# Kernel optimization log

Measured on AMD Instinct MI355X. Metric: run time of the kernel, lower is better.

Reference implementation:

```python
import jax, jax.numpy as jnp
import numpy as np

B, H, W, C, WS, SS = 32, 192, 192, 64, 6, 3
NH, NW = H // WS, W // WS
EPS = 1e-5

def _ln(x, g, b):
    m = x.mean(-1, keepdims=True)
    v = ((x - m) ** 2).mean(-1, keepdims=True)
    return (x - m) * jax.lax.rsqrt(v + EPS) * g + b

def _block(x, Wm, bm, g, b):
    # Linear -> LayerNorm -> GELU (exact erf, matching torch nn.GELU); dropout inactive (eval)
    return jax.nn.gelu(_ln(x @ Wm + bm, g, b), approximate=False)

def _window_context(grid, Wt, bt, gt, bet):
    # partition into WSxWS windows and mean-pool per window: [B,NH,NW,C]
    pooled = grid.reshape(B, NH, WS, NW, WS, C).mean(axis=(2, 4))
    tok = _block(pooled, Wt, bt, gt, bet)           # token_proj
    # broadcast window summary back to pixel grid: [B,H,W,C]
    return jnp.repeat(jnp.repeat(tok, WS, axis=1), WS, axis=2)

def setup_inputs() -> dict:
    key = jax.random.key(0)
    ks = jax.random.split(key, 7)
    return {
        "h_pixel": jax.random.normal(ks[0], (B, H * W, C), jnp.float32),
        "token_W": jax.random.normal(ks[1], (C, C), jnp.float32) * 0.05,
        "token_b": jax.random.normal(ks[2], (C,), jnp.float32) * 0.05,
        "token_g": jnp.ones((C,), jnp.float32),
        "token_beta": jnp.zeros((C,), jnp.float32),
        "fuse_W": jax.random.normal(ks[3], (C, C), jnp.float32) * 0.05,
        "fuse_b": jax.random.normal(ks[4], (C,), jnp.float32) * 0.05,
        "fuse_g": jnp.ones((C,), jnp.float32),
        "fuse_beta": jnp.zeros((C,), jnp.float32),
        "out_W": jax.random.normal(ks[5], (C, C), jnp.float32) * 0.05,
        "out_b": jax.random.normal(ks[6], (C,), jnp.float32) * 0.05,
        "out_g": jnp.ones((C,), jnp.float32),
        "out_beta": jnp.zeros((C,), jnp.float32),
    }

def reference(h_pixel, token_W, token_b, token_g, token_beta,
              fuse_W, fuse_b, fuse_g, fuse_beta,
              out_W, out_b, out_g, out_beta):
    grid = h_pixel.reshape(B, H, W, C)
    reg = _window_context(grid, token_W, token_b, token_g, token_beta)
    shifted = _window_context(jnp.roll(grid, (-SS, -SS), (1, 2)),
                              token_W, token_b, token_g, token_beta)
    shifted = jnp.roll(shifted, (SS, SS), (1, 2))
    ctx = _block(reg + shifted, fuse_W, fuse_b, fuse_g, fuse_beta)   # fuse (sum merge)
    ctx = _block(ctx, out_W, out_b, out_g, out_beta)                 # out_proj
    return ctx.reshape(B, H * W, C)
```

## Files before the change

kernel.cpp:

```cpp
#include <hip/hip_runtime.h>
#include <math.h>


#define HH 192
#define WW 192
#define CC 64

__device__ __forceinline__ float gelu_exact(float x) {
    return 0.5f * x * (1.0f + erff(x * 0.70710678118654752440f));
}

__device__ __forceinline__ float bcast(float v, int k) {
    return __int_as_float(__builtin_amdgcn_readlane(__float_as_int(v), k));
}

__device__ __forceinline__ float matvec64(float m, const float* Wc, float bias) {
    float y0 = bias, y1 = 0.f, y2 = 0.f, y3 = 0.f;
#pragma unroll
    for (int k = 0; k < 64; k += 4) {
        y0 += bcast(m, k)     * Wc[k];
        y1 += bcast(m, k + 1) * Wc[k + 1];
        y2 += bcast(m, k + 2) * Wc[k + 2];
        y3 += bcast(m, k + 3) * Wc[k + 3];
    }
    return (y0 + y1) + (y2 + y3);
}

__device__ __forceinline__ float ln_gelu(float y, float g, float b) {
    float s1 = y, s2 = y * y;
#pragma unroll
    for (int off = 32; off > 0; off >>= 1) {
        s1 += __shfl_xor(s1, off, 64);
        s2 += __shfl_xor(s2, off, 64);
    }
    float m = s1 * (1.0f / 64.0f);
    float v = s2 * (1.0f / 64.0f) - m * m;
    v = v < 0.f ? 0.f : v;
    return gelu_exact((y - m) * rsqrtf(v + 1e-5f) * g + b);
}

extern "C" __global__ __launch_bounds__(256)
void k_blocksum(const float* __restrict__ h, float* __restrict__ S) {
    int bby = blockIdx.x;
    int b = bby >> 6, by = bby & 63;
    for (int item = threadIdx.x; item < 512; item += 256) {
        int bx = item >> 3;
        int c0 = (item & 7) * 8;
        float acc[8] = {0.f, 0.f, 0.f, 0.f, 0.f, 0.f, 0.f, 0.f};
#pragma unroll
        for (int dy = 0; dy < 3; ++dy) {
#pragma unroll
            for (int dx = 0; dx < 3; ++dx) {
                int y = by * 3 + dy, x = bx * 3 + dx;
                const float4* p = reinterpret_cast<const float4*>(
                    h + (((size_t)b * HH + y) * WW + x) * CC + c0);
                float4 v0 = p[0], v1 = p[1];
                acc[0] += v0.x; acc[1] += v0.y; acc[2] += v0.z; acc[3] += v0.w;
                acc[4] += v1.x; acc[5] += v1.y; acc[6] += v1.z; acc[7] += v1.w;
            }
        }
        float4* o = reinterpret_cast<float4*>(S + (((size_t)bby) * 64 + bx) * CC + c0);
        o[0] = make_float4(acc[0], acc[1], acc[2], acc[3]);
        o[1] = make_float4(acc[4], acc[5], acc[6], acc[7]);
    }
}

extern "C" __global__ __launch_bounds__(256)
void k_token(const float* __restrict__ S,
             const float* __restrict__ Wt, const float* __restrict__ bt,
             const float* __restrict__ gt, const float* __restrict__ bet,
             float* __restrict__ tok) {
    int lane = threadIdx.x & 63;
    int wg = blockIdx.x * 4 + (threadIdx.x >> 6);
    float Wc[64];
#pragma unroll
    for (int k = 0; k < 64; ++k) Wc[k] = Wt[k * 64 + lane];
    float bias = bt[lane], gg = gt[lane], bb = bet[lane];
    int row0 = wg * 16;
    for (int i = 0; i < 16; ++i) {
        int row = row0 + i;
        int mode = row >> 15;
        int r = row & 32767;
        int b = r >> 10, wy = (r >> 5) & 31, wx = r & 31;
        int r0, r1, c0, c1;
        if (mode == 0) { r0 = 2 * wy;     r1 = 2 * wy + 1;        c0 = 2 * wx;     c1 = 2 * wx + 1; }
        else           { r0 = 2 * wy + 1; r1 = (2 * wy + 2) & 63; c0 = 2 * wx + 1; c1 = (2 * wx + 2) & 63; }
        const float* Sb = S + (size_t)b * 64 * 64 * 64;
        float pooled = (Sb[(r0 * 64 + c0) * 64 + lane] + Sb[(r0 * 64 + c1) * 64 + lane] +
                        Sb[(r1 * 64 + c0) * 64 + lane] + Sb[(r1 * 64 + c1) * 64 + lane]) * (1.0f / 36.0f);
        float y = matvec64(pooled, Wc, bias);
        tok[(size_t)row * 64 + lane] = ln_gelu(y, gg, bb);
    }
}

extern "C" __global__ __launch_bounds__(256)
void k_fuse(const float* __restrict__ tok,
            const float* __restrict__ Wf, const float* __restrict__ bf_,
            const float* __restrict__ gf, const float* __restrict__ bef,
            float* __restrict__ h1) {
    int lane = threadIdx.x & 63;
    int wg = blockIdx.x * 4 + (threadIdx.x >> 6);
    float Wc[64];
#pragma unroll
    for (int k = 0; k < 64; ++k) Wc[k] = Wf[k * 64 + lane];
    float fb = bf_[lane], fg = gf[lane], fbe = bef[lane];
    int row0 = wg * 16;
    for (int i = 0; i < 16; ++i) {
        int row = row0 + i;
        int b = row >> 12;
        int rem = row & 4095;
        int wy = rem >> 7, wx = (rem >> 2) & 31, q = rem & 3;
        int sy = (wy + 31 + (q >> 1)) & 31;
        int sx = (wx + 31 + (q & 1)) & 31;
        const float* t0 = tok + (size_t)b * 65536;
        const float* t1 = tok + 2097152 + (size_t)b * 65536;
        float m = t0[(wy * 32 + wx) * 64 + lane] + t1[(sy * 32 + sx) * 64 + lane];
        float y = matvec64(m, Wc, fb);
        h1[(size_t)row * 64 + lane] = ln_gelu(y, fg, fbe);
    }
}

extern "C" __global__ __launch_bounds__(256)
void k_outbc(const float* __restrict__ h1,
             const float* __restrict__ Wo, const float* __restrict__ bo_,
             const float* __restrict__ go, const float* __restrict__ beo,
             float* __restrict__ out) {
    int lane = threadIdx.x & 63;
    int wg = blockIdx.x * 4 + (threadIdx.x >> 6);
    float Wc[64];
#pragma unroll
    for (int k = 0; k < 64; ++k) Wc[k] = Wo[k * 64 + lane];
    float ob = bo_[lane], og = go[lane], obe = beo[lane];
    int row0 = wg * 16;
    for (int i = 0; i < 16; ++i) {
        int row = row0 + i;
        float m = h1[(size_t)row * 64 + lane];
        float z = matvec64(m, Wc, ob);
        float o = ln_gelu(z, og, obe);
        int b = row >> 12;
        int rem = row & 4095;
        int wy = rem >> 7, wx = (rem >> 2) & 31, q = rem & 3;
        int y0 = wy * 6 + (q >> 1) * 3;
        int x0 = wx * 6 + (q & 1) * 3;
        float* obase = out + (((size_t)b * HH + y0) * WW + x0) * CC + lane;
#pragma unroll
        for (int dy = 0; dy < 3; ++dy) {
#pragma unroll
            for (int dx = 0; dx < 3; ++dx) {
                obase[((size_t)dy * WW + dx) * CC] = o;
            }
        }
    }
}

extern "C" void kernel_launch(void* const* d_in, const int* in_sizes, int n_in,
                              void* d_out, int out_size, void* d_ws, size_t ws_size,
                              hipStream_t stream) {
    const float* h   = (const float*)d_in[0];
    const float* tW  = (const float*)d_in[1];
    const float* tb  = (const float*)d_in[2];
    const float* tg  = (const float*)d_in[3];
    const float* tbe = (const float*)d_in[4];
    const float* fW  = (const float*)d_in[5];
    const float* fb  = (const float*)d_in[6];
    const float* fg  = (const float*)d_in[7];
    const float* fbe = (const float*)d_in[8];
    const float* oW  = (const float*)d_in[9];
    const float* ob  = (const float*)d_in[10];
    const float* og  = (const float*)d_in[11];
    const float* obe = (const float*)d_in[12];
    float* out = (float*)d_out;

    char* ws = (char*)d_ws;
    float* S   = (float*)(ws);
    float* tok = (float*)(ws + 33554432);
    float* h1  = S;

    hipLaunchKernelGGL(k_blocksum, dim3(2048), dim3(256), 0, stream, h, S);
    hipLaunchKernelGGL(k_token, dim3(1024), dim3(256), 0, stream,
                       S, tW, tb, tg, tbe, tok);
    hipLaunchKernelGGL(k_fuse, dim3(2048), dim3(256), 0, stream,
                       tok, fW, fb, fg, fbe, h1);
    hipLaunchKernelGGL(k_outbc, dim3(2048), dim3(256), 0, stream,
                       h1, oW, ob, og, obe, out);
}
```

Before: 622.2 us.

## Fold LayerNorm mean into centered weights and load activation rows via scalar loads

Adds a prep kernel that subtracts the per-row output-channel mean from each weight matrix and bias. This makes the linear output zero-mean, so LayerNorm only needs the variance reduction and half the cross-lane shuffles go away. The fuse and out kernels now fetch each 64-float input row with s_load_dwordx16 into scalar registers instead of broadcasting with readlane. The fuse kernel also reuses the regular-token partial matvec across the four shifted quadrants. The costs are an extra tiny launch, inline asm with a full lgkmcnt wait per row, and a more serialized scalar-load path.

```diff
diff --git a/kernel.cpp b/kernel.cpp
--- a/kernel.cpp
+++ b/kernel.cpp
@@ -6,12 +6,39 @@
 #define WW 192
 #define CC 64
 
+typedef __attribute__((ext_vector_type(16))) int i16v;
+
 __device__ __forceinline__ float gelu_exact(float x) {
     return 0.5f * x * (1.0f + erff(x * 0.70710678118654752440f));
 }
-
+__device__ __forceinline__ float wsum64(float v) {
+#pragma unroll
+    for (int off = 32; off > 0; off >>= 1) v += __shfl_xor(v, off, 64);
+    return v;
+}
 __device__ __forceinline__ float bcast(float v, int k) {
     return __int_as_float(__builtin_amdgcn_readlane(__float_as_int(v), k));
+}
+
+__device__ __forceinline__ void smem_row64(const float* rp,
+                                           i16v& a, i16v& b, i16v& c, i16v& d) {
+    asm volatile("s_load_dwordx16 %0, %4, 0x0\n\t"
+                 "s_load_dwordx16 %1, %4, 0x40\n\t"
+                 "s_load_dwordx16 %2, %4, 0x80\n\t"
+                 "s_load_dwordx16 %3, %4, 0xc0\n\t"
+                 "s_waitcnt lgkmcnt(0)"
+                 : "=&s"(a), "=&s"(b), "=&s"(c), "=&s"(d)
+                 : "s"(rp));
+}
+__device__ __forceinline__ void mac16(const i16v& a, const float* Wc, int base,
+                                      float& y0, float& y1, float& y2, float& y3) {
+#pragma unroll
+    for (int t = 0; t < 16; t += 4) {
+        y0 = fmaf(__int_as_float(a[t + 0]), Wc[base + t + 0], y0);
+        y1 = fmaf(__int_as_float(a[t + 1]), Wc[base + t + 1], y1);
+        y2 = fmaf(__int_as_float(a[t + 2]), Wc[base + t + 2], y2);
+        y3 = fmaf(__int_as_float(a[t + 3]), Wc[base + t + 3], y3);
+    }
 }
 
 __device__ __forceinline__ float matvec64(float m, const float* Wc, float bias) {
@@ -26,17 +53,31 @@
     return (y0 + y1) + (y2 + y3);
 }
 
-__device__ __forceinline__ float ln_gelu(float y, float g, float b) {
-    float s1 = y, s2 = y * y;
-#pragma unroll
-    for (int off = 32; off > 0; off >>= 1) {
-        s1 += __shfl_xor(s1, off, 64);
-        s2 += __shfl_xor(s2, off, 64);
-    }
-    float m = s1 * (1.0f / 64.0f);
-    float v = s2 * (1.0f / 64.0f) - m * m;
-    v = v < 0.f ? 0.f : v;
-    return gelu_exact((y - m) * rsqrtf(v + 1e-5f) * g + b);
+__device__ __forceinline__ float ln_gelu_c(float y, float g, float b) {
+    float s2 = y * y;
+#pragma unroll
+    for (int off = 32; off > 0; off >>= 1) s2 += __shfl_xor(s2, off, 64);
+    float v = s2 * (1.0f / 64.0f);
+    return gelu_exact(y * rsqrtf(v + 1e-5f) * g + b);
+}
+
+extern "C" __global__ __launch_bounds__(192)
+void k_prep(const float* __restrict__ W0, const float* __restrict__ b0,
+            const float* __restrict__ W1, const float* __restrict__ b1,
+            const float* __restrict__ W2, const float* __restrict__ b2,
+            float* __restrict__ cw) {
+    int lane = threadIdx.x & 63;
+    int w = threadIdx.x >> 6;
+    const float* W  = (w == 0) ? W0 : (w == 1) ? W1 : W2;
+    const float* bs = (w == 0) ? b0 : (w == 1) ? b1 : b2;
+    float* Wo = cw + w * 4096;
+    float* bo = cw + 12288 + w * 64;
+    for (int k = 0; k < 64; ++k) {
+        float v = W[k * 64 + lane];
+        Wo[k * 64 + lane] = v - wsum64(v) * (1.0f / 64.0f);
+    }
+    float bv = bs[lane];
+    bo[lane] = bv - wsum64(bv) * (1.0f / 64.0f);
 }
 
 extern "C" __global__ __launch_bounds__(256)
@@ -89,7 +130,7 @@
         float pooled = (Sb[(r0 * 64 + c0) * 64 + lane] + Sb[(r0 * 64 + c1) * 64 + lane] +
                         Sb[(r1 * 64 + c0) * 64 + lane] + Sb[(r1 * 64 + c1) * 64 + lane]) * (1.0f / 36.0f);
         float y = matvec64(pooled, Wc, bias);
-        tok[(size_t)row * 64 + lane] = ln_gelu(y, gg, bb);
+        tok[(size_t)row * 64 + lane] = ln_gelu_c(y, gg, bb);
     }
 }
 
@@ -99,24 +140,41 @@
             const float* __restrict__ gf, const float* __restrict__ bef,
             float* __restrict__ h1) {
     int lane = threadIdx.x & 63;
-    int wg = blockIdx.x * 4 + (threadIdx.x >> 6);
+    int wid = __builtin_amdgcn_readfirstlane(threadIdx.x >> 6);
+    int wg = blockIdx.x * 4 + wid;
     float Wc[64];
 #pragma unroll
     for (int k = 0; k < 64; ++k) Wc[k] = Wf[k * 64 + lane];
     float fb = bf_[lane], fg = gf[lane], fbe = bef[lane];
     int row0 = wg * 16;
-    for (int i = 0; i < 16; ++i) {
-        int row = row0 + i;
-        int b = row >> 12;
-        int rem = row & 4095;
-        int wy = rem >> 7, wx = (rem >> 2) & 31, q = rem & 3;
-        int sy = (wy + 31 + (q >> 1)) & 31;
-        int sx = (wx + 31 + (q & 1)) & 31;
-        const float* t0 = tok + (size_t)b * 65536;
-        const float* t1 = tok + 2097152 + (size_t)b * 65536;
-        float m = t0[(wy * 32 + wx) * 64 + lane] + t1[(sy * 32 + sx) * 64 + lane];
-        float y = matvec64(m, Wc, fb);
-        h1[(size_t)row * 64 + lane] = ln_gelu(y, fg, fbe);
+    int b = row0 >> 12;
+    int rem = row0 & 4095;
+    int wy = rem >> 7, wx0 = (rem >> 2) & 31;
+    const float* t0 = tok + (size_t)b * 65536;
+    const float* t1 = tok + 2097152 + (size_t)b * 65536;
+    for (int j = 0; j < 4; ++j) {
+        int wx = wx0 + j;
+        i16v a0, a1, a2, a3;
+        smem_row64(t0 + (wy * 32 + wx) * 64, a0, a1, a2, a3);
+        float s0 = fb, s1 = 0.f, s2 = 0.f, s3 = 0.f;
+        mac16(a0, Wc, 0, s0, s1, s2, s3);
+        mac16(a1, Wc, 16, s0, s1, s2, s3);
+        mac16(a2, Wc, 32, s0, s1, s2, s3);
+        mac16(a3, Wc, 48, s0, s1, s2, s3);
+#pragma unroll
+        for (int q = 0; q < 4; ++q) {
+            int sy = (wy + 31 + (q >> 1)) & 31;
+            int sx = (wx + 31 + (q & 1)) & 31;
+            i16v b0, b1, b2, b3;
+            smem_row64(t1 + (sy * 32 + sx) * 64, b0, b1, b2, b3);
+            float y0 = s0, y1 = s1, y2 = s2, y3 = s3;
+            mac16(b0, Wc, 0, y0, y1, y2, y3);
+            mac16(b1, Wc, 16, y0, y1, y2, y3);
+            mac16(b2, Wc, 32, y0, y1, y2, y3);
+            mac16(b3, Wc, 48, y0, y1, y2, y3);
+            float y = (y0 + y1) + (y2 + y3);
+            h1[(size_t)(row0 + j * 4 + q) * 64 + lane] = ln_gelu_c(y, fg, fbe);
+        }
     }
 }
 
@@ -126,7 +184,8 @@
              const float* __restrict__ go, const float* __restrict__ beo,
              float* __restrict__ out) {
     int lane = threadIdx.x & 63;
-    int wg = blockIdx.x * 4 + (threadIdx.x >> 6);
+    int wid = __builtin_amdgcn_readfirstlane(threadIdx.x >> 6);
+    int wg = blockIdx.x * 4 + wid;
     float Wc[64];
 #pragma unroll
     for (int k = 0; k < 64; ++k) Wc[k] = Wo[k * 64 + lane];
@@ -134,15 +193,21 @@
     int row0 = wg * 16;
     for (int i = 0; i < 16; ++i) {
         int row = row0 + i;
-        float m = h1[(size_t)row * 64 + lane];
-        float z = matvec64(m, Wc, ob);
-        float o = ln_gelu(z, og, obe);
+        i16v a0, a1, a2, a3;
+        smem_row64(h1 + (size_t)row * 64, a0, a1, a2, a3);
+        float y0 = ob, y1 = 0.f, y2 = 0.f, y3 = 0.f;
+        mac16(a0, Wc, 0, y0, y1, y2, y3);
+        mac16(a1, Wc, 16, y0, y1, y2, y3);
+        mac16(a2, Wc, 32, y0, y1, y2, y3);
+        mac16(a3, Wc, 48, y0, y1, y2, y3);
+        float y = (y0 + y1) + (y2 + y3);
+        float o = ln_gelu_c(y, og, obe);
         int b = row >> 12;
         int rem = row & 4095;
         int wy = rem >> 7, wx = (rem >> 2) & 31, q = rem & 3;
-        int y0 = wy * 6 + (q >> 1) * 3;
-        int x0 = wx * 6 + (q & 1) * 3;
-        float* obase = out + (((size_t)b * HH + y0) * WW + x0) * CC + lane;
+        int y0p = wy * 6 + (q >> 1) * 3;
+        int x0p = wx * 6 + (q & 1) * 3;
+        float* obase = out + (((size_t)b * HH + y0p) * WW + x0p) * CC + lane;
 #pragma unroll
         for (int dy = 0; dy < 3; ++dy) {
 #pragma unroll
@@ -175,12 +240,17 @@
     float* S   = (float*)(ws);
     float* tok = (float*)(ws + 33554432);
     float* h1  = S;
-
+    float* cw  = (float*)(ws + 67108864);
+    float* Wtc = cw,          *Wfc = cw + 4096, *Woc = cw + 8192;
+    float* btc = cw + 12288,  *bfc = cw + 12352, *boc = cw + 12416;
+
+    hipLaunchKernelGGL(k_prep, dim3(1), dim3(192), 0, stream,
+                       tW, tb, fW, fb, oW, ob, cw);
     hipLaunchKernelGGL(k_blocksum, dim3(2048), dim3(256), 0, stream, h, S);
     hipLaunchKernelGGL(k_token, dim3(1024), dim3(256), 0, stream,
-                       S, tW, tb, tg, tbe, tok);
+                       S, Wtc, btc, tg, tbe, tok);
     hipLaunchKernelGGL(k_fuse, dim3(2048), dim3(256), 0, stream,
-                       tok, fW, fb, fg, fbe, h1);
+                       tok, Wfc, bfc, fg, fbe, h1);
     hipLaunchKernelGGL(k_outbc, dim3(2048), dim3(256), 0, stream,
-                       h1, oW, ob, og, obe, out);
-}
+                       h1, Woc, boc, og, obe, out);
+}
```

New measurement: 631.9 us. No clear change (+1.6%).
